# Performance work log

Hardware: AMD Instinct MI355X
Metric: run time of the kernel (lower is better)

## Reference

```python
import jax, jax.numpy as jnp
import numpy as np

C, H = 256, 8
D = C // H
L, T, R = 2, 2, 3
OUT = 64
N = (30000, 50000)          # (author, paper)
F_IN = (128, 256)
E = (300000, 300000, 400000)
ETYPES = ((0, 1, 0), (1, 0, 1), (1, 1, 2))  # (src_type, dst_type, rel_idx)
SCALE = 1.0 / float(np.sqrt(D))


def setup_inputs() -> dict:
    key = jax.random.key(0)
    ks = iter(jax.random.split(key, 40))
    def nrm(shape, scale):
        return jax.random.normal(next(ks), shape, dtype=jnp.float32) * scale
    inp = {
        "x_author": nrm((N[0], F_IN[0]), 1.0),
        "x_paper": nrm((N[1], F_IN[1]), 1.0),
        "lin_in_author_W": nrm((F_IN[0], C), F_IN[0] ** -0.5),
        "lin_in_author_b": jnp.zeros((C,), jnp.float32),
        "lin_in_paper_W": nrm((F_IN[1], C), F_IN[1] ** -0.5),
        "lin_in_paper_b": jnp.zeros((C,), jnp.float32),
        "k_W": nrm((L, T, C, C), C ** -0.5), "k_b": jnp.zeros((L, T, C), jnp.float32),
        "q_W": nrm((L, T, C, C), C ** -0.5), "q_b": jnp.zeros((L, T, C), jnp.float32),
        "v_W": nrm((L, T, C, C), C ** -0.5), "v_b": jnp.zeros((L, T, C), jnp.float32),
        "a_W": nrm((L, R, H, D, D), D ** -0.5),
        "m_W": nrm((L, R, H, D, D), D ** -0.5),
        "p_rel": jnp.ones((L, R, H), jnp.float32),
        "skip": jnp.ones((L, T), jnp.float32),
        "out_W": nrm((L, T, C, C), C ** -0.5), "out_b": jnp.zeros((L, T, C), jnp.float32),
        "lin_out_W": nrm((C, OUT), C ** -0.5), "lin_out_b": jnp.zeros((OUT,), jnp.float32),
    }
    names = ("ei_writes", "ei_rev_writes", "ei_cites")
    for name, (s, d, _), e in zip(names, ETYPES, E):
        src = jax.random.randint(next(ks), (e,), 0, N[s], dtype=jnp.int32)
        dst = jax.random.randint(next(ks), (e,), 0, N[d], dtype=jnp.int32)
        inp[name] = jnp.stack([src, dst])
    inp["targetnode"] = 0
    return inp


def _seg_softmax(logits, seg, num_segments):
    # numerically stable softmax over ragged groups of edges sharing a dst node
    m = jax.ops.segment_max(logits, seg, num_segments=num_segments)
    m = jnp.where(jnp.isfinite(m), m, 0.0)
    ex = jnp.exp(logits - m[seg])
    s = jax.ops.segment_sum(ex, seg, num_segments=num_segments)
    return ex / (s[seg] + 1e-16)


def _hgt_forward(x_author, x_paper,
                 lin_in_author_W, lin_in_author_b, lin_in_paper_W, lin_in_paper_b,
                 k_W, k_b, q_W, q_b, v_W, v_b, a_W, m_W, p_rel, skip,
                 out_W, out_b, lin_out_W, lin_out_b, eis):
    # per-type input projection + relu
    xs = [
        jax.nn.relu(x_author @ lin_in_author_W + lin_in_author_b),
        jax.nn.relu(x_paper @ lin_in_paper_W + lin_in_paper_b),
    ]
    for l in range(L):
        # per node type k/q/v: [N_t, H, D]
        k = [(xs[t] @ k_W[l, t] + k_b[l, t]).reshape(N[t], H, D) for t in range(T)]
        q = [(xs[t] @ q_W[l, t] + q_b[l, t]).reshape(N[t], H, D) for t in range(T)]
        v = [(xs[t] @ v_W[l, t] + v_b[l, t]).reshape(N[t], H, D) for t in range(T)]
        agg = [jnp.zeros((N[t], H, D), xs[t].dtype) for t in range(T)]
        for (s, d, r), ei in zip(ETYPES, eis):
            src, dst = ei[0], ei[1]
            # relation-specific head-wise transforms of source keys/values
            k_r = jnp.einsum('nhd,hde->nhe', k[s], a_W[l, r])
            v_r = jnp.einsum('nhd,hde->nhe', v[s], m_W[l, r])
            # per-edge attention logits [E, H]
            alpha = jnp.einsum('ehd,ehd->eh', q[d][dst], k_r[src]) * p_rel[l, r] * SCALE
            w = _seg_softmax(alpha, dst, N[d])
            agg[d] = agg[d] + jax.ops.segment_sum(v_r[src] * w[..., None], dst,
                                                  num_segments=N[d])
        new_xs = []
        for t in range(T):
            o = jax.nn.gelu(agg[t].reshape(N[t], C)) @ out_W[l, t] + out_b[l, t]
            beta = jax.nn.sigmoid(skip[l, t])
            new_xs.append(beta * o + (1.0 - beta) * xs[t])
        xs = new_xs
    # shared output linear per node type
    return tuple(x @ lin_out_W + lin_out_b for x in xs)


def reference(x_author, x_paper, lin_in_author_W, lin_in_author_b,
              lin_in_paper_W, lin_in_paper_b, k_W, k_b, q_W, q_b, v_W, v_b,
              a_W, m_W, p_rel, skip, out_W, out_b, lin_out_W, lin_out_b,
              ei_writes, ei_rev_writes, ei_cites, targetnode):
    eis = (ei_writes, ei_rev_writes, ei_cites)
    return _hgt_forward(x_author, x_paper,
                        lin_in_author_W, lin_in_author_b,
                        lin_in_paper_W, lin_in_paper_b,
                        k_W, k_b, q_W, q_b, v_W, v_b, a_W, m_W, p_rel, skip,
                        out_W, out_b, lin_out_W, lin_out_b, eis)
```

## Files before the change

kernel.cpp:

```cpp
#include <hip/hip_runtime.h>


#define CC 256
#define HH 8
#define DD 32
#define LL 2
#define TT 2
#define RR 3
#define OUTD 64

typedef unsigned short bf16_t;
struct us4 { unsigned short x, y, z, w; };
typedef __attribute__((ext_vector_type(8))) short short8;
typedef __attribute__((ext_vector_type(4))) float f32x4;

__device__ __forceinline__ float b2f(unsigned short u) {
  return __uint_as_float(((unsigned)u) << 16);
}
__device__ __forceinline__ float blo(unsigned u) {
  return __uint_as_float(u << 16);
}
__device__ __forceinline__ float bhi(unsigned u) {
  return __uint_as_float(u & 0xFFFF0000u);
}
__device__ __forceinline__ unsigned short f2b(float f) {
  unsigned u = __float_as_uint(f);
  unsigned r = (u + 0x7FFFu + ((u >> 16) & 1u)) >> 16;
  return (unsigned short)r;
}
__device__ __forceinline__ float ld_dyn(const void* p, size_t e, bool isb) {
  return isb ? b2f(((const bf16_t*)p)[e]) : ((const float*)p)[e];
}
__device__ __forceinline__ float4 load4_dyn(const void* p, size_t e, bool isb) {
  if (isb) {
    us4 v = *(const us4*)((const bf16_t*)p + e);
    return make_float4(b2f(v.x), b2f(v.y), b2f(v.z), b2f(v.w));
  }
  return *(const float4*)((const float*)p + e);
}
__device__ __forceinline__ void st_dyn(void* p, size_t e, float v, bool isb) {
  if (isb) ((bf16_t*)p)[e] = f2b(v);
  else ((float*)p)[e] = v;
}
__device__ __forceinline__ float gelu1(float v) {
  const float t = tanhf(0.7978845608028654f * (v + 0.044715f * v * v * v));
  return 0.5f * v * (1.f + t);
}

__global__ void detect_kernel(const unsigned* __restrict__ probe,
                              int* __restrict__ flag) {
  *flag = (*probe == 0x3F800000u) ? 0 : 1;
}

__global__ __launch_bounds__(256) void prep_kernel(
    const void* __restrict__ xA, const void* __restrict__ xP,
    const void* __restrict__ WinA, const void* __restrict__ WinP,
    const void* __restrict__ qW, const void* __restrict__ outW,
    const void* __restrict__ binA, const void* __restrict__ binP,
    const void* __restrict__ qb, const void* __restrict__ ob,
    bf16_t* __restrict__ dq0, bf16_t* __restrict__ dq1,
    bf16_t* __restrict__ dWinAt, bf16_t* __restrict__ dWinPt,
    bf16_t* __restrict__ dqWt, bf16_t* __restrict__ doutWt,
    float* __restrict__ dbinA, float* __restrict__ dbinP,
    float* __restrict__ dqb, float* __restrict__ dob,
    int* __restrict__ zbase, int zn, int N0, int N1,
    const int* __restrict__ dflag) {
  const bool isb = (*dflag != 0);
  int gid = blockIdx.x * 256 + threadIdx.x;
  const int n0 = N0 * 128, n1 = N1 * 256;
  if (gid < n0) { dq0[gid] = f2b(ld_dyn(xA, gid, isb)); return; }
  gid -= n0;
  if (gid < n1) { dq1[gid] = f2b(ld_dyn(xP, gid, isb)); return; }
  gid -= n1;
  if (gid < 128 * 256) {
    const int n = gid % 256, k = gid / 256;
    dWinAt[n * 128 + k] = f2b(ld_dyn(WinA, gid, isb));
    return;
  }
  gid -= 128 * 256;
  if (gid < 256 * 256) {
    const int n = gid % 256, k = gid / 256;
    dWinPt[n * 256 + k] = f2b(ld_dyn(WinP, gid, isb));
    return;
  }
  gid -= 256 * 256;
  if (gid < 4 * 65536) {
    const int lt = gid >> 16, i = gid & 65535;
    const int n = i % 256, k = i / 256;
    dqWt[(size_t)lt * 65536 + n * 256 + k] =
        f2b(ld_dyn(qW, (size_t)lt * 65536 + i, isb));
    return;
  }
  gid -= 4 * 65536;
  if (gid < 4 * 65536) {
    const int lt = gid >> 16, i = gid & 65535;
    const int n = i % 256, k = i / 256;
    doutWt[(size_t)lt * 65536 + n * 256 + k] =
        f2b(ld_dyn(outW, (size_t)lt * 65536 + i, isb));
    return;
  }
  gid -= 4 * 65536;
  if (gid < 256) { dbinA[gid] = ld_dyn(binA, gid, isb); return; }
  gid -= 256;
  if (gid < 256) { dbinP[gid] = ld_dyn(binP, gid, isb); return; }
  gid -= 256;
  if (gid < 1024) { dqb[gid] = ld_dyn(qb, gid, isb); return; }
  gid -= 1024;
  if (gid < 1024) { dob[gid] = ld_dyn(ob, gid, isb); return; }
  gid -= 1024;
  if (gid < zn) zbase[gid] = 0;
}

__global__ __launch_bounds__(256) void fuse_w_kernel(
    const void* __restrict__ kW, const void* __restrict__ vW,
    const void* __restrict__ kb, const void* __restrict__ vb,
    const void* __restrict__ aW, const void* __restrict__ mW,
    bf16_t* __restrict__ Wcat, float* __restrict__ bcat,
    const int* __restrict__ dflag) {
  const bool isb = (*dflag != 0);
  const int lr = blockIdx.x;
  const int l = lr / RR;
  const int r = lr % RR;
  const int which = blockIdx.y;
  const int h = blockIdx.z;
  const int srct[RR] = {0, 1, 1};
  const int s = srct[r];
  __shared__ float Amat[DD][DD];
  const void* Ap = (which == 0 ? aW : mW);
  const size_t Apoff = (size_t)(lr * HH + h) * DD * DD;
  for (int i = threadIdx.x; i < DD * DD; i += 256)
    Amat[i / DD][i % DD] = ld_dyn(Ap, Apoff + i, isb);
  __syncthreads();
  const void* Wsrc = (which == 0 ? kW : vW);
  const void* bsrc = (which == 0 ? kb : vb);
  const size_t Wsoff = (size_t)(l * TT + s) * CC * CC;
  const size_t bsoff = (size_t)(l * TT + s) * CC;
  bf16_t* Wt = Wcat + (size_t)lr * 512 * CC;
  float* bdst = bcat + (size_t)lr * 512;
  const int c = threadIdx.x;
  float wrow[DD];
#pragma unroll
  for (int d = 0; d < DD; ++d)
    wrow[d] = ld_dyn(Wsrc, Wsoff + (size_t)c * CC + h * DD + d, isb);
#pragma unroll 4
  for (int e = 0; e < DD; ++e) {
    float acc = 0.f;
#pragma unroll
    for (int d = 0; d < DD; ++d) acc += wrow[d] * Amat[d][e];
    const int clo = h * DD + e;
    const int phys = ((clo >> 2) << 3) + (which << 2) + (clo & 3);
    Wt[(size_t)phys * CC + c] = f2b(acc);
  }
  if (c < DD) {
    float acc = 0.f;
#pragma unroll
    for (int d = 0; d < DD; ++d)
      acc += ld_dyn(bsrc, bsoff + h * DD + d, isb) * Amat[d][c];
    const int clo = h * DD + c;
    const int phys = ((clo >> 2) << 3) + (which << 2) + (clo & 3);
    bdst[phys] = acc;
  }
}

template <int EPI>
__global__ __launch_bounds__(256) void mgemm_kernel(
    const bf16_t* __restrict__ A, const bf16_t* __restrict__ Bt,
    const float* __restrict__ bias, const bf16_t* __restrict__ Sold,
    const void* __restrict__ skipv, int skipIdx, bf16_t* __restrict__ Cm,
    int M, int N, int K, const int* __restrict__ dflag) {
  __shared__ bf16_t Asb[128][72];
  __shared__ bf16_t Bsb[128][72];
  const int bm = blockIdx.x * 128;
  const int bn = blockIdx.y * 128;
  const int tid = threadIdx.x;
  const int wave = tid >> 6;
  const int lane = tid & 63;
  const int qd = lane >> 4;
  const int l16 = lane & 15;
  const int wm = (wave & 1) * 64;
  const int wn = (wave >> 1) * 64;
  f32x4 acc[4][4] = {};
  for (int k0 = 0; k0 < K; k0 += 64) {
#pragma unroll
    for (int i = 0; i < 4; ++i) {
      const int c = tid + 256 * i;
      const int row = c >> 3;
      const int col = (c & 7) * 8;
      uint4 va = make_uint4(0u, 0u, 0u, 0u);
      if (bm + row < M)
        va = *(const uint4*)(A + (size_t)(bm + row) * K + k0 + col);
      *(uint4*)&Asb[row][col] = va;
      const uint4 vb = *(const uint4*)(Bt + (size_t)(bn + row) * K + k0 + col);
      *(uint4*)&Bsb[row][col] = vb;
    }
    __syncthreads();
#pragma unroll
    for (int s = 0; s < 2; ++s) {
      short8 af[4], bf[4];
#pragma unroll
      for (int i = 0; i < 4; ++i) {
        af[i] = *(const short8*)&Asb[wm + i * 16 + l16][s * 32 + qd * 8];
        bf[i] = *(const short8*)&Bsb[wn + i * 16 + l16][s * 32 + qd * 8];
      }
#pragma unroll
      for (int mi = 0; mi < 4; ++mi)
#pragma unroll
        for (int ni = 0; ni < 4; ++ni)
          acc[mi][ni] = __builtin_amdgcn_mfma_f32_16x16x32_bf16(
              af[mi], bf[ni], acc[mi][ni], 0, 0, 0);
    }
    __syncthreads();
  }
  float beta = 0.f;
  if (EPI == 2) beta = 1.f / (1.f + __expf(-ld_dyn(skipv, skipIdx, *dflag != 0)));
#pragma unroll
  for (int mi = 0; mi < 4; ++mi) {
#pragma unroll
    for (int r = 0; r < 4; ++r) {
      const int row = bm + wm + mi * 16 + qd * 4 + r;
      if (row < M) {
#pragma unroll
        for (int ni = 0; ni < 4; ++ni) {
          const int col = bn + wn + ni * 16 + l16;
          float v = acc[mi][ni][r] + bias[col];
          if (EPI == 1) v = fmaxf(v, 0.f);
          if (EPI == 2)
            v = beta * v + (1.f - beta) * b2f(Sold[(size_t)row * N + col]);
          Cm[(size_t)row * N + col] = f2b(v);
        }
      }
    }
  }
}

__global__ __launch_bounds__(256) void fgemm_kernel(
    const bf16_t* __restrict__ A, const void* __restrict__ B,
    const void* __restrict__ bias, void* __restrict__ Cm, size_t Coff, int M,
    int N, int K, const int* __restrict__ dflag) {
  const bool isb = (*dflag != 0);
  __shared__ float As[32][68];
  __shared__ float Bs[32][64];
  const int bm = blockIdx.x * 64;
  const int tid = threadIdx.x;
  const int tx = tid & 15;
  const int ty = tid >> 4;
  float acc[4][4] = {};
  for (int k0 = 0; k0 < K; k0 += 32) {
    {
      const int r = tid >> 3;
      const int c4 = (tid & 7) << 2;
#pragma unroll
      for (int rr = 0; rr < 2; ++rr) {
        const int row = bm + r + rr * 32;
        float4 v = make_float4(0.f, 0.f, 0.f, 0.f);
        if (row < M) v = load4_dyn(A, (size_t)row * K + k0 + c4, true);
        As[c4 + 0][r + rr * 32] = v.x;
        As[c4 + 1][r + rr * 32] = v.y;
        As[c4 + 2][r + rr * 32] = v.z;
        As[c4 + 3][r + rr * 32] = v.w;
      }
    }
    {
      const int r = tid >> 4;
      const int c4 = (tid & 15) << 2;
#pragma unroll
      for (int rr = 0; rr < 2; ++rr) {
        const float4 v = load4_dyn(B, (size_t)(k0 + r + rr * 16) * N + c4, isb);
        *(float4*)&Bs[r + rr * 16][c4] = v;
      }
    }
    __syncthreads();
#pragma unroll
    for (int kk = 0; kk < 32; ++kk) {
      const float4 av = *(const float4*)&As[kk][ty << 2];
      const float4 bv = *(const float4*)&Bs[kk][tx << 2];
      acc[0][0] += av.x * bv.x; acc[0][1] += av.x * bv.y;
      acc[0][2] += av.x * bv.z; acc[0][3] += av.x * bv.w;
      acc[1][0] += av.y * bv.x; acc[1][1] += av.y * bv.y;
      acc[1][2] += av.y * bv.z; acc[1][3] += av.y * bv.w;
      acc[2][0] += av.z * bv.x; acc[2][1] += av.z * bv.y;
      acc[2][2] += av.z * bv.z; acc[2][3] += av.z * bv.w;
      acc[3][0] += av.w * bv.x; acc[3][1] += av.w * bv.y;
      acc[3][2] += av.w * bv.z; acc[3][3] += av.w * bv.w;
    }
    __syncthreads();
  }
#pragma unroll
  for (int i = 0; i < 4; ++i) {
    const int row = bm + (ty << 2) + i;
    if (row < M) {
#pragma unroll
      for (int j = 0; j < 4; ++j) {
        const int col = (tx << 2) + j;
        const float v = acc[i][j] + ld_dyn(bias, col, isb);
        st_dyn(Cm, Coff + (size_t)row * N + col, v, isb);
      }
    }
  }
}

__global__ void countA_kernel(const int* __restrict__ e0, int E0,
                              const int* __restrict__ e1, int E1,
                              const int* __restrict__ e2, int E2,
                              int* __restrict__ c0, int* __restrict__ c1,
                              int* __restrict__ c2) {
  int g = blockIdx.x * 256 + threadIdx.x;
  if (g < E0) { atomicAdd(&c0[e0[E0 + g]], 1); return; }
  g -= E0;
  if (g < E1) { atomicAdd(&c1[e1[E1 + g]], 1); return; }
  g -= E1;
  if (g < E2) atomicAdd(&c2[e2[E2 + g]], 1);
}

__global__ __launch_bounds__(256) void scan1A_kernel(
    const int* __restrict__ c0, int n0_, const int* __restrict__ c1, int n1_,
    const int* __restrict__ c2, int n2_, int* __restrict__ bsum, int nch0,
    int nch1) {
  int b = blockIdx.x;
  const int* c;
  int n, rel;
  if (b < nch0) { rel = 0; c = c0; n = n0_; }
  else if (b < nch0 + nch1) { rel = 1; c = c1; n = n1_; b -= nch0; }
  else { rel = 2; c = c2; n = n2_; b -= nch0 + nch1; }
  const int base = b * 1024;
  int s = 0;
#pragma unroll
  for (int j = 0; j < 4; ++j) {
    const int i = base + threadIdx.x + j * 256;
    s += (i < n) ? c[i] : 0;
  }
  __shared__ int red[256];
  red[threadIdx.x] = s;
  __syncthreads();
  for (int d = 128; d > 0; d >>= 1) {
    if (threadIdx.x < d) red[threadIdx.x] += red[threadIdx.x + d];
    __syncthreads();
  }
  if (threadIdx.x == 0) bsum[rel * 64 + b] = red[0];
}

__global__ __launch_bounds__(64) void scan2A_kernel(int* __restrict__ bsum,
                                                    int* __restrict__ totals,
                                                    int nch0, int nch1,
                                                    int nch2) {
  if (threadIdx.x != 0) return;
  const int rel = blockIdx.x;
  const int nch = (rel == 0) ? nch0 : (rel == 1) ? nch1 : nch2;
  int* bs = bsum + rel * 64;
  int run = 0;
  for (int i = 0; i < nch; ++i) {
    const int v = bs[i];
    bs[i] = run;
    run += v;
  }
  totals[rel] = run;
}

__global__ __launch_bounds__(256) void scan3A_kernel(
    const int* __restrict__ c0, int n0_, const int* __restrict__ c1, int n1_,
    const int* __restrict__ c2, int n2_, const int* __restrict__ bsum,
    const int* __restrict__ totals, int* __restrict__ ip0,
    int* __restrict__ ip1, int* __restrict__ ip2, int nch0, int nch1) {
  int b = blockIdx.x;
  const int* c;
  int* ip;
  int n, rel;
  if (b < nch0) { rel = 0; c = c0; n = n0_; ip = ip0; }
  else if (b < nch0 + nch1) { rel = 1; c = c1; n = n1_; ip = ip1; b -= nch0; }
  else { rel = 2; c = c2; n = n2_; ip = ip2; b -= nch0 + nch1; }
  const int base = b * 1024;
  int v[4];
  int s = 0;
#pragma unroll
  for (int j = 0; j < 4; ++j) {
    const int i = base + threadIdx.x * 4 + j;
    v[j] = (i < n) ? c[i] : 0;
    s += v[j];
  }
  __shared__ int ts[256];
  ts[threadIdx.x] = s;
  __syncthreads();
  for (int d = 1; d < 256; d <<= 1) {
    const int t = (threadIdx.x >= d) ? ts[threadIdx.x - d] : 0;
    __syncthreads();
    ts[threadIdx.x] += t;
    __syncthreads();
  }
  int run = bsum[rel * 64 + b] + ((threadIdx.x > 0) ? ts[threadIdx.x - 1] : 0);
#pragma unroll
  for (int j = 0; j < 4; ++j) {
    const int i = base + threadIdx.x * 4 + j;
    if (i < n) ip[i] = run;
    run += v[j];
  }
  if (b == 0 && threadIdx.x == 0) ip[n] = totals[rel];
}

__global__ void fillA_kernel(const int* __restrict__ e0, int E0,
                             const int* __restrict__ e1, int E1,
                             const int* __restrict__ e2, int E2,
                             const int* __restrict__ ip0,
                             const int* __restrict__ ip1,
                             const int* __restrict__ ip2, int* __restrict__ u0,
                             int* __restrict__ u1, int* __restrict__ u2,
                             int* __restrict__ s0, int* __restrict__ s1,
                             int* __restrict__ s2) {
  int g = blockIdx.x * 256 + threadIdx.x;
  const int* ei;
  const int* ip;
  int* cur;
  int* srcs;
  int E;
  if (g < E0) { ei = e0; E = E0; ip = ip0; cur = u0; srcs = s0; }
  else {
    g -= E0;
    if (g < E1) { ei = e1; E = E1; ip = ip1; cur = u1; srcs = s1; }
    else {
      g -= E1;
      if (g >= E2) return;
      ei = e2; E = E2; ip = ip2; cur = u2; srcs = s2;
    }
  }
  const int d = ei[E + g];
  const int pos = ip[d] + atomicAdd(&cur[d], 1);
  srcs[pos] = ei[g];
}

template <int NREL>
__global__ __launch_bounds__(256) void aggf3_kernel(
    const bf16_t* __restrict__ q, const uint4* __restrict__ kv0,
    const int* __restrict__ ip0, const int* __restrict__ ss0, int po0,
    const uint4* __restrict__ kv1, const int* __restrict__ ip1,
    const int* __restrict__ ss1, int po1, const void* __restrict__ prel,
    float scale, bf16_t* __restrict__ outb, int Nd,
    const int* __restrict__ dflag) {
  const bool isb = (*dflag != 0);
  const int d = blockIdx.x * 4 + (threadIdx.x >> 6);
  if (d >= Nd) return;
  const int lane = threadIdx.x & 63;
  const int hM = lane >> 3;
  const us4 qv = ((const us4*)q)[(size_t)d * 64 + lane];
  const float q0 = b2f(qv.x), q1 = b2f(qv.y), q2 = b2f(qv.z), q3 = b2f(qv.w);
  float a0 = 0.f, a1 = 0.f, a2 = 0.f, a3 = 0.f;

#define LDBLK(P, X0, X1, X2, X3)                       \
  {                                                    \
    const int pm_ = p1v - 1;                           \
    int i1_ = (P) + 1, i2_ = (P) + 2, i3_ = (P) + 3;   \
    i1_ = i1_ > pm_ ? pm_ : i1_;                       \
    i2_ = i2_ > pm_ ? pm_ : i2_;                       \
    i3_ = i3_ > pm_ ? pm_ : i3_;                       \
    X0 = kv[(size_t)ss[(P)] * 64 + lane];              \
    X1 = kv[(size_t)ss[i1_] * 64 + lane];              \
    X2 = kv[(size_t)ss[i2_] * 64 + lane];              \
    X3 = kv[(size_t)ss[i3_] * 64 + lane];              \
  }

#define CPTBLK(P, X0, X1, X2, X3)                                             \
  {                                                                           \
    float t0 = q0 * blo(X0.x) + q1 * bhi(X0.x) + q2 * blo(X0.y) + q3 * bhi(X0.y); \
    float t1 = q0 * blo(X1.x) + q1 * bhi(X1.x) + q2 * blo(X1.y) + q3 * bhi(X1.y); \
    float t2 = q0 * blo(X2.x) + q1 * bhi(X2.x) + q2 * blo(X2.y) + q3 * bhi(X2.y); \
    float t3 = q0 * blo(X3.x) + q1 * bhi(X3.x) + q2 * blo(X3.y) + q3 * bhi(X3.y); \
    t0 += __shfl_xor(t0, 1, 8); t1 += __shfl_xor(t1, 1, 8);                   \
    t2 += __shfl_xor(t2, 1, 8); t3 += __shfl_xor(t3, 1, 8);                   \
    t0 += __shfl_xor(t0, 2, 8); t1 += __shfl_xor(t1, 2, 8);                   \
    t2 += __shfl_xor(t2, 2, 8); t3 += __shfl_xor(t3, 2, 8);                   \
    t0 += __shfl_xor(t0, 4, 8); t1 += __shfl_xor(t1, 4, 8);                   \
    t2 += __shfl_xor(t2, 4, 8); t3 += __shfl_xor(t3, 4, 8);                   \
    float l0 = t0 * ph, l1 = t1 * ph, l2 = t2 * ph, l3 = t3 * ph;             \
    const int rem_ = p1v - (P);                                               \
    if (rem_ < 4) {                                                           \
      if (rem_ <= 1) l1 = -1.0e38f;                                           \
      if (rem_ <= 2) l2 = -1.0e38f;                                           \
      l3 = -1.0e38f;                                                          \
    }                                                                         \
    const float mn = fmaxf(fmaxf(fmaxf(l0, l1), fmaxf(l2, l3)), m);           \
    const float sc = __expf(m - mn);                                          \
    const float w0 = __expf(l0 - mn);                                         \
    const float w1 = __expf(l1 - mn);                                         \
    const float w2 = __expf(l2 - mn);                                         \
    const float w3 = __expf(l3 - mn);                                         \
    lsum = lsum * sc + (w0 + w1 + w2 + w3);                                   \
    b0 = b0 * sc + w0 * blo(X0.z) + w1 * blo(X1.z) + w2 * blo(X2.z) + w3 * blo(X3.z); \
    b1 = b1 * sc + w0 * bhi(X0.z) + w1 * bhi(X1.z) + w2 * bhi(X2.z) + w3 * bhi(X3.z); \
    b2 = b2 * sc + w0 * blo(X0.w) + w1 * blo(X1.w) + w2 * blo(X2.w) + w3 * blo(X3.w); \
    b3 = b3 * sc + w0 * bhi(X0.w) + w1 * bhi(X1.w) + w2 * bhi(X2.w) + w3 * bhi(X3.w); \
    m = mn;                                                                   \
  }

#pragma unroll
  for (int rel = 0; rel < NREL; ++rel) {
    const uint4* kv = rel ? kv1 : kv0;
    const int* ip = rel ? ip1 : ip0;
    const int* ss = rel ? ss1 : ss0;
    const float ph = ld_dyn(prel, (rel ? po1 : po0) + hM, isb) * scale;
    const int p0v = ip[d];
    const int p1v = ip[d + 1];
    if (p0v == p1v) continue;
    float m = -3.0e38f, lsum = 0.f;
    float b0 = 0.f, b1 = 0.f, b2 = 0.f, b3 = 0.f;
    uint4 A0, A1, A2, A3, B0, B1, B2, B3;
    int p = p0v;
    LDBLK(p, A0, A1, A2, A3);
    for (;;) {
      if (p + 4 < p1v) LDBLK(p + 4, B0, B1, B2, B3);
      CPTBLK(p, A0, A1, A2, A3);
      p += 4;
      if (p >= p1v) break;
      if (p + 4 < p1v) LDBLK(p + 4, A0, A1, A2, A3);
      CPTBLK(p, B0, B1, B2, B3);
      p += 4;
      if (p >= p1v) break;
    }
    const float inv = 1.f / (lsum + 1e-16f);
    a0 += b0 * inv;
    a1 += b1 * inv;
    a2 += b2 * inv;
    a3 += b3 * inv;
  }
#undef LDBLK
#undef CPTBLK
  us4 r;
  r.x = f2b(gelu1(a0));
  r.y = f2b(gelu1(a1));
  r.z = f2b(gelu1(a2));
  r.w = f2b(gelu1(a3));
  ((us4*)outb)[(size_t)d * 64 + lane] = r;
}

extern "C" void kernel_launch(void* const* d_in, const int* in_sizes, int n_in,
                              void* d_out, int out_size, void* d_ws,
                              size_t ws_size, hipStream_t stream) {
  const void* xA = d_in[0];
  const void* xP = d_in[1];
  const void* WinA = d_in[2];
  const void* binA = d_in[3];
  const void* WinP = d_in[4];
  const void* binP = d_in[5];
  const void* kW = d_in[6];
  const void* kb = d_in[7];
  const void* qW = d_in[8];
  const void* qb = d_in[9];
  const void* vW = d_in[10];
  const void* vb = d_in[11];
  const void* aW = d_in[12];
  const void* mW = d_in[13];
  const void* prel = d_in[14];
  const void* skipv = d_in[15];
  const void* outW = d_in[16];
  const void* outb = d_in[17];
  const void* WoutL = d_in[18];
  const void* boutL = d_in[19];
  const int* eiA[RR] = {(const int*)d_in[20], (const int*)d_in[21],
                        (const int*)d_in[22]};
  const int Ecnt[RR] = {in_sizes[20] / 2, in_sizes[21] / 2, in_sizes[22] / 2};
  const int N0 = in_sizes[0] / 128;
  const int N1 = in_sizes[1] / 256;
  const int Nn[TT] = {N0, N1};
  const float SCALE = 0.17677669529663687f;
  (void)n_in; (void)out_size; (void)ws_size;

  float* w = (float*)d_ws;
  size_t off = 0;
  auto alloc = [&](size_t nf) { float* p = w + off; off += (nf + 3) & ~3ull; return p; };
  int* dflag = (int*)alloc(4);
  bf16_t* xsb[TT];
  xsb[0] = (bf16_t*)alloc((size_t)N0 * CC / 2);
  xsb[1] = (bf16_t*)alloc((size_t)N1 * CC / 2);
  bf16_t* qbuf[TT];
  qbuf[0] = (bf16_t*)alloc((size_t)N0 * CC / 2);
  qbuf[1] = (bf16_t*)alloc((size_t)N1 * CC / 2);
  bf16_t* buf_a = (bf16_t*)alloc((size_t)N0 * 512 / 2);
  bf16_t* buf_p = (bf16_t*)alloc((size_t)N1 * 512 / 2);
  bf16_t* Wcat = (bf16_t*)alloc((size_t)LL * RR * 512 * CC / 2);
  float* bcat = alloc((size_t)LL * RR * 512);
  bf16_t* qWt = (bf16_t*)alloc((size_t)LL * TT * CC * CC / 2);
  bf16_t* outWt = (bf16_t*)alloc((size_t)LL * TT * CC * CC / 2);
  bf16_t* WinAt = (bf16_t*)alloc((size_t)CC * 128 / 2);
  bf16_t* WinPt = (bf16_t*)alloc((size_t)CC * CC / 2);
  float* binAf = alloc(CC);
  float* binPf = alloc(CC);
  float* qbf = alloc((size_t)LL * TT * CC);
  float* outbf = alloc((size_t)LL * TT * CC);
  int* indptr[RR];
  int* srcs[RR];
  for (int r = 0; r < RR; ++r) {
    const int nd = (r == 1) ? N0 : N1;
    indptr[r] = (int*)alloc((size_t)nd + 1);
    srcs[r] = (int*)alloc((size_t)Ecnt[r]);
  }
  const int zn = 2 * (2 * N1 + N0);
  int* cntall = (int*)alloc((size_t)zn);
  int* cnt0 = cntall;           int* cur0 = cnt0 + N1;
  int* cnt1 = cur0 + N1;        int* cur1 = cnt1 + N0;
  int* cnt2 = cur1 + N0;        int* cur2 = cnt2 + N1;
  int* bsum = (int*)alloc(3 * 64);
  int* stotal = (int*)alloc(4);

  detect_kernel<<<1, 1, 0, stream>>>((const unsigned*)skipv, dflag);

  {
    const size_t total = (size_t)N0 * 128 + (size_t)N1 * 256 + 128 * 256 +
                         256 * 256 + 4 * 65536 + 4 * 65536 + 256 + 256 + 1024 +
                         1024 + zn;
    prep_kernel<<<(int)((total + 255) / 256), 256, 0, stream>>>(
        xA, xP, WinA, WinP, qW, outW, binA, binP, qb, outb, qbuf[0], qbuf[1],
        WinAt, WinPt, qWt, outWt, binAf, binPf, qbf, outbf, cntall, zn, N0, N1,
        dflag);
  }
  fuse_w_kernel<<<dim3(LL * RR, 2, HH), 256, 0, stream>>>(
      kW, vW, kb, vb, aW, mW, Wcat, bcat, dflag);

  {
    const int E0 = Ecnt[0], E1 = Ecnt[1], E2 = Ecnt[2];
    const int nch0 = (N1 + 1023) / 1024;
    const int nch1 = (N0 + 1023) / 1024;
    const int nch2 = (N1 + 1023) / 1024;
    const int EG = (E0 + E1 + E2 + 255) / 256;
    countA_kernel<<<EG, 256, 0, stream>>>(eiA[0], E0, eiA[1], E1, eiA[2], E2,
                                          cnt0, cnt1, cnt2);
    scan1A_kernel<<<nch0 + nch1 + nch2, 256, 0, stream>>>(
        cnt0, N1, cnt1, N0, cnt2, N1, bsum, nch0, nch1);
    scan2A_kernel<<<3, 64, 0, stream>>>(bsum, stotal, nch0, nch1, nch2);
    scan3A_kernel<<<nch0 + nch1 + nch2, 256, 0, stream>>>(
        cnt0, N1, cnt1, N0, cnt2, N1, bsum, stotal, indptr[0], indptr[1],
        indptr[2], nch0, nch1);
    fillA_kernel<<<EG, 256, 0, stream>>>(eiA[0], E0, eiA[1], E1, eiA[2], E2,
                                         indptr[0], indptr[1], indptr[2], cur0,
                                         cur1, cur2, srcs[0], srcs[1], srcs[2]);
  }

  mgemm_kernel<1><<<dim3((N0 + 127) / 128, 2), 256, 0, stream>>>(
      qbuf[0], WinAt, binAf, nullptr, nullptr, 0, xsb[0], N0, CC, 128, dflag);
  mgemm_kernel<1><<<dim3((N1 + 127) / 128, 2), 256, 0, stream>>>(
      qbuf[1], WinPt, binPf, nullptr, nullptr, 0, xsb[1], N1, CC, 256, dflag);

  const int mbA = (N0 + 127) / 128;
  const int mbP = (N1 + 127) / 128;
  for (int l = 0; l < LL; ++l) {
    const int lt0 = l * TT + 0, lt1 = l * TT + 1;
    const int lr0 = l * RR + 0, lr1 = l * RR + 1, lr2 = l * RR + 2;
    mgemm_kernel<0><<<dim3(mbA, 2), 256, 0, stream>>>(
        xsb[0], qWt + (size_t)lt0 * CC * CC, qbf + (size_t)lt0 * CC, nullptr,
        nullptr, 0, qbuf[0], N0, CC, CC, dflag);
    mgemm_kernel<0><<<dim3(mbP, 2), 256, 0, stream>>>(
        xsb[1], qWt + (size_t)lt1 * CC * CC, qbf + (size_t)lt1 * CC, nullptr,
        nullptr, 0, qbuf[1], N1, CC, CC, dflag);
    mgemm_kernel<0><<<dim3(mbP, 4), 256, 0, stream>>>(
        xsb[1], Wcat + (size_t)lr1 * 512 * CC, bcat + (size_t)lr1 * 512,
        nullptr, nullptr, 0, buf_p, N1, 512, CC, dflag);
    aggf3_kernel<1><<<(N0 + 3) / 4, 256, 0, stream>>>(
        qbuf[0], (const uint4*)buf_p, indptr[1], srcs[1], lr1 * HH, nullptr,
        nullptr, nullptr, 0, prel, SCALE, qbuf[0], N0, dflag);
    mgemm_kernel<0><<<dim3(mbA, 4), 256, 0, stream>>>(
        xsb[0], Wcat + (size_t)lr0 * 512 * CC, bcat + (size_t)lr0 * 512,
        nullptr, nullptr, 0, buf_a, N0, 512, CC, dflag);
    mgemm_kernel<0><<<dim3(mbP, 4), 256, 0, stream>>>(
        xsb[1], Wcat + (size_t)lr2 * 512 * CC, bcat + (size_t)lr2 * 512,
        nullptr, nullptr, 0, buf_p, N1, 512, CC, dflag);
    aggf3_kernel<2><<<(N1 + 3) / 4, 256, 0, stream>>>(
        qbuf[1], (const uint4*)buf_a, indptr[0], srcs[0], lr0 * HH,
        (const uint4*)buf_p, indptr[2], srcs[2], lr2 * HH, prel, SCALE, qbuf[1],
        N1, dflag);
    mgemm_kernel<2><<<dim3(mbA, 2), 256, 0, stream>>>(
        qbuf[0], outWt + (size_t)lt0 * CC * CC, outbf + (size_t)lt0 * CC,
        xsb[0], skipv, lt0, xsb[0], N0, CC, CC, dflag);
    mgemm_kernel<2><<<dim3(mbP, 2), 256, 0, stream>>>(
        qbuf[1], outWt + (size_t)lt1 * CC * CC, outbf + (size_t)lt1 * CC,
        xsb[1], skipv, lt1, xsb[1], N1, CC, CC, dflag);
  }

  fgemm_kernel<<<dim3((N0 + 63) / 64), 256, 0, stream>>>(
      xsb[0], WoutL, boutL, d_out, 0, N0, OUTD, CC, dflag);
  fgemm_kernel<<<dim3((N1 + 63) / 64), 256, 0, stream>>>(
      xsb[1], WoutL, boutL, d_out, (size_t)N0 * OUTD, N1, OUTD, CC, dflag);
}
```

Measured before the change: 1.213 ms.

## Prefetch next K-tile into registers in mgemm and swap grid order for row reuse

```diff
diff --git a/kernel.cpp b/kernel.cpp
--- a/kernel.cpp
+++ b/kernel.cpp
@@ -170,8 +170,8 @@
     int M, int N, int K, const int* __restrict__ dflag) {
   __shared__ bf16_t Asb[128][72];
   __shared__ bf16_t Bsb[128][72];
-  const int bm = blockIdx.x * 128;
-  const int bn = blockIdx.y * 128;
+  const int bm = blockIdx.y * 128;
+  const int bn = blockIdx.x * 128;
   const int tid = threadIdx.x;
   const int wave = tid >> 6;
   const int lane = tid & 63;
@@ -180,20 +180,37 @@
   const int wm = (wave & 1) * 64;
   const int wn = (wave >> 1) * 64;
   f32x4 acc[4][4] = {};
+  uint4 ra[4], rb[4];
+
+#define MG_LOADT(K0)                                                       \
+  {                                                                        \
+    _Pragma("unroll") for (int i = 0; i < 4; ++i) {                        \
+      const int c = tid + 256 * i;                                         \
+      const int row = c >> 3;                                              \
+      const int col = (c & 7) * 8;                                         \
+      ra[i] = make_uint4(0u, 0u, 0u, 0u);                                  \
+      if (bm + row < M)                                                    \
+        ra[i] = *(const uint4*)(A + (size_t)(bm + row) * K + (K0) + col);  \
+      rb[i] = *(const uint4*)(Bt + (size_t)(bn + row) * K + (K0) + col);   \
+    }                                                                      \
+  }
+#define MG_STORET()                                                        \
+  {                                                                        \
+    _Pragma("unroll") for (int i = 0; i < 4; ++i) {                        \
+      const int c = tid + 256 * i;                                         \
+      const int row = c >> 3;                                              \
+      const int col = (c & 7) * 8;                                         \
+      *(uint4*)&Asb[row][col] = ra[i];                                     \
+      *(uint4*)&Bsb[row][col] = rb[i];                                     \
+    }                                                                      \
+  }
+
+  MG_LOADT(0);
+  MG_STORET();
+  __syncthreads();
   for (int k0 = 0; k0 < K; k0 += 64) {
-#pragma unroll
-    for (int i = 0; i < 4; ++i) {
-      const int c = tid + 256 * i;
-      const int row = c >> 3;
-      const int col = (c & 7) * 8;
-      uint4 va = make_uint4(0u, 0u, 0u, 0u);
-      if (bm + row < M)
-        va = *(const uint4*)(A + (size_t)(bm + row) * K + k0 + col);
-      *(uint4*)&Asb[row][col] = va;
-      const uint4 vb = *(const uint4*)(Bt + (size_t)(bn + row) * K + k0 + col);
-      *(uint4*)&Bsb[row][col] = vb;
-    }
-    __syncthreads();
+    const bool more = (k0 + 64) < K;
+    if (more) MG_LOADT(k0 + 64);
 #pragma unroll
     for (int s = 0; s < 2; ++s) {
       short8 af[4], bf[4];
@@ -210,7 +227,13 @@
               af[mi], bf[ni], acc[mi][ni], 0, 0, 0);
     }
     __syncthreads();
-  }
+    if (more) {
+      MG_STORET();
+      __syncthreads();
+    }
+  }
+#undef MG_LOADT
+#undef MG_STORET
   float beta = 0.f;
   if (EPI == 2) beta = 1.f / (1.f + __expf(-ld_dyn(skipv, skipIdx, *dflag != 0)));
 #pragma unroll
@@ -631,9 +654,9 @@
                                          cur1, cur2, srcs[0], srcs[1], srcs[2]);
   }
 
-  mgemm_kernel<1><<<dim3((N0 + 127) / 128, 2), 256, 0, stream>>>(
+  mgemm_kernel<1><<<dim3(2, (N0 + 127) / 128), 256, 0, stream>>>(
       qbuf[0], WinAt, binAf, nullptr, nullptr, 0, xsb[0], N0, CC, 128, dflag);
-  mgemm_kernel<1><<<dim3((N1 + 127) / 128, 2), 256, 0, stream>>>(
+  mgemm_kernel<1><<<dim3(2, (N1 + 127) / 128), 256, 0, stream>>>(
       qbuf[1], WinPt, binPf, nullptr, nullptr, 0, xsb[1], N1, CC, 256, dflag);
 
   const int mbA = (N0 + 127) / 128;
@@ -641,32 +664,32 @@
   for (int l = 0; l < LL; ++l) {
     const int lt0 = l * TT + 0, lt1 = l * TT + 1;
     const int lr0 = l * RR + 0, lr1 = l * RR + 1, lr2 = l * RR + 2;
-    mgemm_kernel<0><<<dim3(mbA, 2), 256, 0, stream>>>(
+    mgemm_kernel<0><<<dim3(2, mbA), 256, 0, stream>>>(
         xsb[0], qWt + (size_t)lt0 * CC * CC, qbf + (size_t)lt0 * CC, nullptr,
         nullptr, 0, qbuf[0], N0, CC, CC, dflag);
-    mgemm_kernel<0><<<dim3(mbP, 2), 256, 0, stream>>>(
+    mgemm_kernel<0><<<dim3(2, mbP), 256, 0, stream>>>(
         xsb[1], qWt + (size_t)lt1 * CC * CC, qbf + (size_t)lt1 * CC, nullptr,
         nullptr, 0, qbuf[1], N1, CC, CC, dflag);
-    mgemm_kernel<0><<<dim3(mbP, 4), 256, 0, stream>>>(
+    mgemm_kernel<0><<<dim3(4, mbP), 256, 0, stream>>>(
         xsb[1], Wcat + (size_t)lr1 * 512 * CC, bcat + (size_t)lr1 * 512,
         nullptr, nullptr, 0, buf_p, N1, 512, CC, dflag);
     aggf3_kernel<1><<<(N0 + 3) / 4, 256, 0, stream>>>(
         qbuf[0], (const uint4*)buf_p, indptr[1], srcs[1], lr1 * HH, nullptr,
         nullptr, nullptr, 0, prel, SCALE, qbuf[0], N0, dflag);
-    mgemm_kernel<0><<<dim3(mbA, 4), 256, 0, stream>>>(
+    mgemm_kernel<0><<<dim3(4, mbA), 256, 0, stream>>>(
         xsb[0], Wcat + (size_t)lr0 * 512 * CC, bcat + (size_t)lr0 * 512,
         nullptr, nullptr, 0, buf_a, N0, 512, CC, dflag);
-    mgemm_kernel<0><<<dim3(mbP, 4), 256, 0, stream>>>(
+    mgemm_kernel<0><<<dim3(4, mbP), 256, 0, stream>>>(
         xsb[1], Wcat + (size_t)lr2 * 512 * CC, bcat + (size_t)lr2 * 512,
         nullptr, nullptr, 0, buf_p, N1, 512, CC, dflag);
     aggf3_kernel<2><<<(N1 + 3) / 4, 256, 0, stream>>>(
         qbuf[1], (const uint4*)buf_a, indptr[0], srcs[0], lr0 * HH,
         (const uint4*)buf_p, indptr[2], srcs[2], lr2 * HH, prel, SCALE, qbuf[1],
         N1, dflag);
-    mgemm_kernel<2><<<dim3(mbA, 2), 256, 0, stream>>>(
+    mgemm_kernel<2><<<dim3(2, mbA), 256, 0, stream>>>(
         qbuf[0], outWt + (size_t)lt0 * CC * CC, outbf + (size_t)lt0 * CC,
         xsb[0], skipv, lt0, xsb[0], N0, CC, CC, dflag);
-    mgemm_kernel<2><<<dim3(mbP, 2), 256, 0, stream>>>(
+    mgemm_kernel<2><<<dim3(2, mbP), 256, 0, stream>>>(
         qbuf[1], outWt + (size_t)lt1 * CC * CC, outbf + (size_t)lt1 * CC,
         xsb[1], skipv, lt1, xsb[1], N1, CC, CC, dflag);
   }
```

Measured after the change: 1.386 ms. 1.14x slower.

## Batch independent GEMMs into grouped launches with segment table

Applied to the files above, without the earlier changes.

```diff
diff --git a/kernel.cpp b/kernel.cpp
--- a/kernel.cpp
+++ b/kernel.cpp
@@ -162,16 +162,39 @@
   }
 }
 
-template <int EPI>
-__global__ __launch_bounds__(256) void mgemm_kernel(
-    const bf16_t* __restrict__ A, const bf16_t* __restrict__ Bt,
-    const float* __restrict__ bias, const bf16_t* __restrict__ Sold,
-    const void* __restrict__ skipv, int skipIdx, bf16_t* __restrict__ Cm,
-    int M, int N, int K, const int* __restrict__ dflag) {
+struct GSeg {
+  const bf16_t* A;
+  const bf16_t* Bt;
+  const float* bias;
+  const bf16_t* Sold;
+  bf16_t* C;
+  int M, N, K, epi, skipIdx, nbx, blk0;
+};
+struct GBatch {
+  GSeg s[6];
+  int nseg;
+};
+
+__global__ __launch_bounds__(256) void bgemm_kernel(
+    GBatch gb, const void* __restrict__ skipv, const int* __restrict__ dflag) {
   __shared__ bf16_t Asb[128][72];
   __shared__ bf16_t Bsb[128][72];
-  const int bm = blockIdx.x * 128;
-  const int bn = blockIdx.y * 128;
+  int si = 0;
+#pragma unroll
+  for (int t = 1; t < 6; ++t)
+    if (t < gb.nseg && (int)blockIdx.x >= gb.s[t].blk0) si = t;
+  const bf16_t* __restrict__ A = gb.s[si].A;
+  const bf16_t* __restrict__ Bt = gb.s[si].Bt;
+  const float* __restrict__ bias = gb.s[si].bias;
+  const bf16_t* __restrict__ Sold = gb.s[si].Sold;
+  bf16_t* __restrict__ Cm = gb.s[si].C;
+  const int M = gb.s[si].M;
+  const int N = gb.s[si].N;
+  const int K = gb.s[si].K;
+  const int epi = gb.s[si].epi;
+  const int local = (int)blockIdx.x - gb.s[si].blk0;
+  const int bn = (local % gb.s[si].nbx) * 128;
+  const int bm = (local / gb.s[si].nbx) * 128;
   const int tid = threadIdx.x;
   const int wave = tid >> 6;
   const int lane = tid & 63;
@@ -212,7 +235,8 @@
     __syncthreads();
   }
   float beta = 0.f;
-  if (EPI == 2) beta = 1.f / (1.f + __expf(-ld_dyn(skipv, skipIdx, *dflag != 0)));
+  if (epi == 2)
+    beta = 1.f / (1.f + __expf(-ld_dyn(skipv, gb.s[si].skipIdx, *dflag != 0)));
 #pragma unroll
   for (int mi = 0; mi < 4; ++mi) {
 #pragma unroll
@@ -223,8 +247,8 @@
         for (int ni = 0; ni < 4; ++ni) {
           const int col = bn + wn + ni * 16 + l16;
           float v = acc[mi][ni][r] + bias[col];
-          if (EPI == 1) v = fmaxf(v, 0.f);
-          if (EPI == 2)
+          if (epi == 1) v = fmaxf(v, 0.f);
+          if (epi == 2)
             v = beta * v + (1.f - beta) * b2f(Sold[(size_t)row * N + col]);
           Cm[(size_t)row * N + col] = f2b(v);
         }
@@ -233,19 +257,27 @@
   }
 }
 
-__global__ __launch_bounds__(256) void fgemm_kernel(
-    const bf16_t* __restrict__ A, const void* __restrict__ B,
-    const void* __restrict__ bias, void* __restrict__ Cm, size_t Coff, int M,
-    int N, int K, const int* __restrict__ dflag) {
+__global__ __launch_bounds__(256) void fgemm2_kernel(
+    const bf16_t* __restrict__ A0, int M0, const bf16_t* __restrict__ A1,
+    int M1, const void* __restrict__ B, const void* __restrict__ bias,
+    void* __restrict__ Cm, const int* __restrict__ dflag) {
   const bool isb = (*dflag != 0);
   __shared__ float As[32][68];
   __shared__ float Bs[32][64];
-  const int bm = blockIdx.x * 64;
+  const int nb0 = (M0 + 63) / 64;
+  const bf16_t* A;
+  int M, bm;
+  size_t Coff;
+  if ((int)blockIdx.x < nb0) {
+    A = A0; M = M0; Coff = 0; bm = blockIdx.x * 64;
+  } else {
+    A = A1; M = M1; Coff = (size_t)M0 * OUTD; bm = (blockIdx.x - nb0) * 64;
+  }
   const int tid = threadIdx.x;
   const int tx = tid & 15;
   const int ty = tid >> 4;
   float acc[4][4] = {};
-  for (int k0 = 0; k0 < K; k0 += 32) {
+  for (int k0 = 0; k0 < CC; k0 += 32) {
     {
       const int r = tid >> 3;
       const int c4 = (tid & 7) << 2;
@@ -253,7 +285,7 @@
       for (int rr = 0; rr < 2; ++rr) {
         const int row = bm + r + rr * 32;
         float4 v = make_float4(0.f, 0.f, 0.f, 0.f);
-        if (row < M) v = load4_dyn(A, (size_t)row * K + k0 + c4, true);
+        if (row < M) v = load4_dyn(A, (size_t)row * CC + k0 + c4, true);
         As[c4 + 0][r + rr * 32] = v.x;
         As[c4 + 1][r + rr * 32] = v.y;
         As[c4 + 2][r + rr * 32] = v.z;
@@ -265,7 +297,8 @@
       const int c4 = (tid & 15) << 2;
 #pragma unroll
       for (int rr = 0; rr < 2; ++rr) {
-        const float4 v = load4_dyn(B, (size_t)(k0 + r + rr * 16) * N + c4, isb);
+        const float4 v =
+            load4_dyn(B, (size_t)(k0 + r + rr * 16) * OUTD + c4, isb);
         *(float4*)&Bs[r + rr * 16][c4] = v;
       }
     }
@@ -293,7 +326,7 @@
       for (int j = 0; j < 4; ++j) {
         const int col = (tx << 2) + j;
         const float v = acc[i][j] + ld_dyn(bias, col, isb);
-        st_dyn(Cm, Coff + (size_t)row * N + col, v, isb);
+        st_dyn(Cm, Coff + (size_t)row * OUTD + col, v, isb);
       }
     }
   }
@@ -557,9 +590,8 @@
   const int Ecnt[RR] = {in_sizes[20] / 2, in_sizes[21] / 2, in_sizes[22] / 2};
   const int N0 = in_sizes[0] / 128;
   const int N1 = in_sizes[1] / 256;
-  const int Nn[TT] = {N0, N1};
   const float SCALE = 0.17677669529663687f;
-  (void)n_in; (void)out_size; (void)ws_size;
+  (void)n_in; (void)out_size;
 
   float* w = (float*)d_ws;
   size_t off = 0;
@@ -597,6 +629,9 @@
   int* cnt2 = cur1 + N0;        int* cur2 = cnt2 + N1;
   int* bsum = (int*)alloc(3 * 64);
   int* stotal = (int*)alloc(4);
+  bf16_t* buf_p2 = (bf16_t*)alloc((size_t)N1 * 512 / 2);
+  const bool haveP2 = (off * 4) <= ws_size;
+  if (!haveP2) buf_p2 = buf_p;
 
   detect_kernel<<<1, 1, 0, stream>>>((const unsigned*)skipv, dflag);
 
@@ -631,48 +666,79 @@
                                          cur1, cur2, srcs[0], srcs[1], srcs[2]);
   }
 
-  mgemm_kernel<1><<<dim3((N0 + 127) / 128, 2), 256, 0, stream>>>(
-      qbuf[0], WinAt, binAf, nullptr, nullptr, 0, xsb[0], N0, CC, 128, dflag);
-  mgemm_kernel<1><<<dim3((N1 + 127) / 128, 2), 256, 0, stream>>>(
-      qbuf[1], WinPt, binPf, nullptr, nullptr, 0, xsb[1], N1, CC, 256, dflag);
-
-  const int mbA = (N0 + 127) / 128;
-  const int mbP = (N1 + 127) / 128;
+  auto launch_batch = [&](GBatch& gb) {
+    int tot = 0;
+    for (int i = 0; i < gb.nseg; ++i) {
+      gb.s[i].nbx = gb.s[i].N / 128;
+      gb.s[i].blk0 = tot;
+      tot += gb.s[i].nbx * ((gb.s[i].M + 127) / 128);
+    }
+    bgemm_kernel<<<tot, 256, 0, stream>>>(gb, skipv, dflag);
+  };
+  auto seg = [](const bf16_t* A, const bf16_t* Bt, const float* bias,
+                const bf16_t* Sold, bf16_t* C, int M, int N, int K, int epi,
+                int skipIdx) {
+    GSeg s;
+    s.A = A; s.Bt = Bt; s.bias = bias; s.Sold = Sold; s.C = C;
+    s.M = M; s.N = N; s.K = K; s.epi = epi; s.skipIdx = skipIdx;
+    s.nbx = 0; s.blk0 = 0;
+    return s;
+  };
+
+  {
+    GBatch b{};
+    b.s[0] = seg(qbuf[1], WinPt, binPf, nullptr, xsb[1], N1, CC, 256, 1, 0);
+    b.s[1] = seg(qbuf[0], WinAt, binAf, nullptr, xsb[0], N0, CC, 128, 1, 0);
+    b.nseg = 2;
+    launch_batch(b);
+  }
+
   for (int l = 0; l < LL; ++l) {
     const int lt0 = l * TT + 0, lt1 = l * TT + 1;
     const int lr0 = l * RR + 0, lr1 = l * RR + 1, lr2 = l * RR + 2;
-    mgemm_kernel<0><<<dim3(mbA, 2), 256, 0, stream>>>(
-        xsb[0], qWt + (size_t)lt0 * CC * CC, qbf + (size_t)lt0 * CC, nullptr,
-        nullptr, 0, qbuf[0], N0, CC, CC, dflag);
-    mgemm_kernel<0><<<dim3(mbP, 2), 256, 0, stream>>>(
-        xsb[1], qWt + (size_t)lt1 * CC * CC, qbf + (size_t)lt1 * CC, nullptr,
-        nullptr, 0, qbuf[1], N1, CC, CC, dflag);
-    mgemm_kernel<0><<<dim3(mbP, 4), 256, 0, stream>>>(
-        xsb[1], Wcat + (size_t)lr1 * 512 * CC, bcat + (size_t)lr1 * 512,
-        nullptr, nullptr, 0, buf_p, N1, 512, CC, dflag);
+    {
+      GBatch b{};
+      int n = 0;
+      b.s[n++] = seg(xsb[1], Wcat + (size_t)lr1 * 512 * CC,
+                     bcat + (size_t)lr1 * 512, nullptr, buf_p, N1, 512, CC, 0, 0);
+      if (haveP2)
+        b.s[n++] = seg(xsb[1], Wcat + (size_t)lr2 * 512 * CC,
+                       bcat + (size_t)lr2 * 512, nullptr, buf_p2, N1, 512, CC,
+                       0, 0);
+      b.s[n++] = seg(xsb[0], Wcat + (size_t)lr0 * 512 * CC,
+                     bcat + (size_t)lr0 * 512, nullptr, buf_a, N0, 512, CC, 0, 0);
+      b.s[n++] = seg(xsb[1], qWt + (size_t)lt1 * CC * CC,
+                     qbf + (size_t)lt1 * CC, nullptr, qbuf[1], N1, CC, CC, 0, 0);
+      b.s[n++] = seg(xsb[0], qWt + (size_t)lt0 * CC * CC,
+                     qbf + (size_t)lt0 * CC, nullptr, qbuf[0], N0, CC, CC, 0, 0);
+      b.nseg = n;
+      launch_batch(b);
+    }
     aggf3_kernel<1><<<(N0 + 3) / 4, 256, 0, stream>>>(
         qbuf[0], (const uint4*)buf_p, indptr[1], srcs[1], lr1 * HH, nullptr,
         nullptr, nullptr, 0, prel, SCALE, qbuf[0], N0, dflag);
-    mgemm_kernel<0><<<dim3(mbA, 4), 256, 0, stream>>>(
-        xsb[0], Wcat + (size_t)lr0 * 512 * CC, bcat + (size_t)lr0 * 512,
-        nullptr, nullptr, 0, buf_a, N0, 512, CC, dflag);
-    mgemm_kernel<0><<<dim3(mbP, 4), 256, 0, stream>>>(
-        xsb[1], Wcat + (size_t)lr2 * 512 * CC, bcat + (size_t)lr2 * 512,
-        nullptr, nullptr, 0, buf_p, N1, 512, CC, dflag);
+    if (!haveP2) {
+      GBatch b{};
+      b.s[0] = seg(xsb[1], Wcat + (size_t)lr2 * 512 * CC,
+                   bcat + (size_t)lr2 * 512, nullptr, buf_p, N1, 512, CC, 0, 0);
+      b.nseg = 1;
+      launch_batch(b);
+    }
     aggf3_kernel<2><<<(N1 + 3) / 4, 256, 0, stream>>>(
         qbuf[1], (const uint4*)buf_a, indptr[0], srcs[0], lr0 * HH,
-        (const uint4*)buf_p, indptr[2], srcs[2], lr2 * HH, prel, SCALE, qbuf[1],
-        N1, dflag);
-    mgemm_kernel<2><<<dim3(mbA, 2), 256, 0, stream>>>(
-        qbuf[0], outWt + (size_t)lt0 * CC * CC, outbf + (size_t)lt0 * CC,
-        xsb[0], skipv, lt0, xsb[0], N0, CC, CC, dflag);
-    mgemm_kernel<2><<<dim3(mbP, 2), 256, 0, stream>>>(
-        qbuf[1], outWt + (size_t)lt1 * CC * CC, outbf + (size_t)lt1 * CC,
-        xsb[1], skipv, lt1, xsb[1], N1, CC, CC, dflag);
-  }
-
-  fgemm_kernel<<<dim3((N0 + 63) / 64), 256, 0, stream>>>(
-      xsb[0], WoutL, boutL, d_out, 0, N0, OUTD, CC, dflag);
-  fgemm_kernel<<<dim3((N1 + 63) / 64), 256, 0, stream>>>(
-      xsb[1], WoutL, boutL, d_out, (size_t)N0 * OUTD, N1, OUTD, CC, dflag);
-}
+        (const uint4*)buf_p2, indptr[2], srcs[2], lr2 * HH, prel, SCALE,
+        qbuf[1], N1, dflag);
+    {
+      GBatch b{};
+      b.s[0] = seg(qbuf[1], outWt + (size_t)lt1 * CC * CC,
+                   outbf + (size_t)lt1 * CC, xsb[1], xsb[1], N1, CC, CC, 2, lt1);
+      b.s[1] = seg(qbuf[0], outWt + (size_t)lt0 * CC * CC,
+                   outbf + (size_t)lt0 * CC, xsb[0], xsb[0], N0, CC, CC, 2, lt0);
+      b.nseg = 2;
+      launch_batch(b);
+    }
+  }
+
+  fgemm2_kernel<<<(N0 + 63) / 64 + (N1 + 63) / 64, 256, 0, stream>>>(
+      xsb[0], N0, xsb[1], N1, WoutL, boutL, d_out, dflag);
+}
```

After: 1.187 ms. 1.02x faster.
